# Kernel optimization log

Hardware: AMD Instinct MI355X
Metric: run time of the kernel (lower is better)

## Reference

```python
import jax, jax.numpy as jnp
import numpy as np

# Mamba3/SSD selective state-space mixer (scalar-A-per-head SSD recurrence,
# causal depthwise conv on x/B/C, gated RMSNorm, in/out projections).
D_MODEL = 1024
EXPAND = 2
D_INNER = EXPAND * D_MODEL            # 2048
HEADDIM = D_MODEL // 16               # 64  (head_count=16 -> headdim 64)
NHEADS = D_INNER // HEADDIM           # 32
D_STATE = 128
CONV_W = 4
CONV_DIM = D_INNER + 2 * D_STATE      # x, B, C share the conv
D_IN_PROJ = 2 * D_INNER + 2 * D_STATE + NHEADS  # z, x, B, C, dt
EPS = 1e-5


def setup_inputs() -> dict:
    key = jax.random.key(0)
    ks = jax.random.split(key, 8)
    B, L = 4, 2048
    hidden = jax.random.normal(ks[0], (B, L, D_MODEL), dtype=jnp.float32)
    W_in = jax.random.normal(ks[1], (D_MODEL, D_IN_PROJ), dtype=jnp.float32) * 0.02
    conv_w = jax.random.normal(ks[2], (CONV_DIM, CONV_W), dtype=jnp.float32) * 0.2
    conv_b = jnp.zeros((CONV_DIM,), dtype=jnp.float32)
    # dt_bias: inverse-softplus of dt ~ U[1e-3, 0.1]
    dt = jnp.exp(jax.random.uniform(ks[3], (NHEADS,)) * (np.log(0.1) - np.log(1e-3)) + np.log(1e-3))
    dt_bias = dt + jnp.log(-jnp.expm1(-dt))
    A_log = jnp.log(jax.random.uniform(ks[4], (NHEADS,), minval=1.0, maxval=16.0))
    D = jnp.ones((NHEADS,), dtype=jnp.float32)
    norm_w = jnp.ones((D_INNER,), dtype=jnp.float32)
    W_out = jax.random.normal(ks[5], (D_INNER, D_MODEL), dtype=jnp.float32) * 0.02
    return {"hidden": hidden, "W_in": W_in, "conv_w": conv_w, "conv_b": conv_b,
            "dt_bias": dt_bias, "A_log": A_log, "D": D, "norm_w": norm_w, "W_out": W_out}


def _silu(x):
    return x * jax.nn.sigmoid(x)


def _mixer(hidden, W_in, conv_w, conv_b, dt_bias, A_log, D, norm_w, W_out):
    Bsz, L, _ = hidden.shape
    zxbcdt = hidden @ W_in                                    # [B,L,D_IN_PROJ]
    z = zxbcdt[..., :D_INNER]
    xBC = zxbcdt[..., D_INNER:D_INNER + CONV_DIM]
    dt = zxbcdt[..., -NHEADS:]                                # [B,L,H]
    # causal depthwise conv, width 4 (small fixed loop over taps)
    xp = jnp.pad(xBC, ((0, 0), (CONV_W - 1, 0), (0, 0)))
    conv = sum(xp[:, k:k + L, :] * conv_w[:, k] for k in range(CONV_W))
    xBC = _silu(conv + conv_b)
    x = xBC[..., :D_INNER].reshape(Bsz, L, NHEADS, HEADDIM)   # [B,L,H,P]
    Bm = xBC[..., D_INNER:D_INNER + D_STATE]                  # [B,L,N]
    Cm = xBC[..., D_INNER + D_STATE:]                         # [B,L,N]
    dt = jax.nn.softplus(dt + dt_bias)                        # [B,L,H]
    dA = jnp.exp(dt * (-jnp.exp(A_log)))                      # [B,L,H] decay in (0,1)
    dBx = jnp.einsum('blh,bln,blhp->blhpn', dt, Bm, x)        # [B,L,H,P,N]

    def step(h, inp):
        dA_t, dBx_t, C_t = inp                                # [B,H],[B,H,P,N],[B,N]
        h = dA_t[:, :, None, None] * h + dBx_t
        y = jnp.einsum('bhpn,bn->bhp', h, C_t)
        return h, y

    h0 = jnp.zeros((Bsz, NHEADS, HEADDIM, D_STATE), dtype=hidden.dtype)
    xs = (jnp.moveaxis(dA, 1, 0), jnp.moveaxis(dBx, 1, 0), jnp.moveaxis(Cm, 1, 0))
    _, ys = jax.lax.scan(step, h0, xs)                        # [L,B,H,P]
    y = jnp.moveaxis(ys, 0, 1) + D[None, None, :, None] * x   # skip term
    y = y.reshape(Bsz, L, D_INNER)
    # gated RMSNorm: norm(y * silu(z))
    y = y * _silu(z)
    y = y * jax.lax.rsqrt(jnp.mean(y * y, axis=-1, keepdims=True) + EPS) * norm_w
    return y @ W_out


def reference(hidden, W_in, conv_w, conv_b, dt_bias, A_log, D, norm_w, W_out):
    return _mixer(hidden, W_in, conv_w, conv_b, dt_bias, A_log, D, norm_w, W_out)
```

## Files before the change

### kernel.cpp

```cpp
#include <hip/hip_runtime.h>
#include <math.h>

#define BSZ 4
#define LEN 2048
#define DM 1024
#define DI 2048
#define HD 64
#define NH 32
#define DS 128
#define CD 2304
#define DP 4384
#define NTOK (BSZ*LEN)
#define QCH 128
#define NCH (LEN/QCH)
#define TOFF (DP-NH)

#define CONV_R 64
#define NRB (NTOK/CONV_R)
#define NPAD 4352

typedef unsigned short ushort_t;
typedef __bf16 bf16x8 __attribute__((ext_vector_type(8)));
typedef ushort_t us8 __attribute__((ext_vector_type(8)));
typedef float f32x4 __attribute__((ext_vector_type(4)));

__device__ __forceinline__ ushort_t f2bf(float f) {
    unsigned u = __float_as_uint(f);
    unsigned r = (u + 0x7FFFu + ((u >> 16) & 1u)) >> 16;
    return (ushort_t)r;
}
__device__ __forceinline__ float bf2f(ushort_t u) {
    return __uint_as_float(((unsigned)u) << 16);
}
__device__ __forceinline__ bf16x8 us2bf(us8 v) {
    union { us8 u; bf16x8 b; } x; x.u = v; return x.b;
}

__device__ __forceinline__ void gl_lds16(const void* g, void* l) {
    __builtin_amdgcn_global_load_lds(
        (const __attribute__((address_space(1))) void*)g,
        (__attribute__((address_space(3))) void*)l, 16, 0, 0);
}

__global__ __launch_bounds__(256) void cvt_bf16(
    const float* __restrict__ A, ushort_t* __restrict__ Ab)
{
    size_t i = ((size_t)blockIdx.x * 256 + threadIdx.x) * 4;
    float4 v = *(const float4*)(A + i);
    ushort_t o[4] = { f2bf(v.x), f2bf(v.y), f2bf(v.z), f2bf(v.w) };
    *(uint2*)(Ab + i) = *(uint2*)o;
}

__global__ __launch_bounds__(256) void transpose_cvt(
    const float* __restrict__ W, ushort_t* __restrict__ Wt,
    const float* __restrict__ colscale, int K, int N, int ldw)
{
    __shared__ float T[32][33];
    const int n0 = blockIdx.x * 32;
    const int k0 = blockIdx.y * 32;
    const int tid = threadIdx.x;
    #pragma unroll
    for (int l = 0; l < 4; l++) {
        int idx = tid + l * 256;
        int ki = idx >> 5, nj = idx & 31;
        int n = n0 + nj;
        float s = colscale ? colscale[k0 + ki] : 1.f;
        T[ki][nj] = (n < N) ? W[(size_t)(k0 + ki) * ldw + n] * s : 0.f;
    }
    __syncthreads();
    #pragma unroll
    for (int l = 0; l < 4; l++) {
        int idx = tid + l * 256;
        int nj = idx >> 5, ki = idx & 31;
        Wt[(size_t)(n0 + nj) * K + k0 + ki] = f2bf(T[ki][nj]);
    }
}

template <bool OB>
__global__ __launch_bounds__(256) void gemm_bf16(
    const ushort_t* __restrict__ A, const ushort_t* __restrict__ Bt,
    void* __restrict__ Cp, const float* __restrict__ rowscale,
    int K, int lda, int ldb, int ldc, int nmax)
{
    __shared__ __align__(16) ushort_t As[128 * 32];
    __shared__ __align__(16) ushort_t Bs[128 * 32];
    const int tid = threadIdx.x;
    int bid = blockIdx.y * gridDim.x + blockIdx.x;
    const int nwg = gridDim.x * gridDim.y;
    if (!(nwg & 7)) bid = (bid & 7) * (nwg >> 3) + (bid >> 3);
    const int n0 = (bid % gridDim.x) * 128;
    const int m0 = (bid / gridDim.x) * 128;
    const int lane = tid & 63;
    const int w = tid >> 6;
    const int wm = w >> 1, wn = w & 1;
    const int lm = lane & 15, quad = lane >> 4;

    const int srow = tid >> 2;
    const int skq = (tid & 3) * 8;
    const ushort_t* ga0 = A + (size_t)(m0 + srow) * lda + skq;
    const ushort_t* ga1 = A + (size_t)(m0 + 64 + srow) * lda + skq;
    const ushort_t* gb0 = Bt + (size_t)(n0 + srow) * ldb + skq;
    const ushort_t* gb1 = Bt + (size_t)(n0 + 64 + srow) * ldb + skq;
    ushort_t* la0 = &As[srow * 32 + skq];
    ushort_t* la1 = &As[(64 + srow) * 32 + skq];
    ushort_t* lb0 = &Bs[srow * 32 + skq];
    ushort_t* lb1 = &Bs[(64 + srow) * 32 + skq];

    f32x4 acc[4][4];
    #pragma unroll
    for (int i = 0; i < 4; i++)
        #pragma unroll
        for (int j = 0; j < 4; j++) acc[i][j] = (f32x4){0.f, 0.f, 0.f, 0.f};

    for (int k0 = 0; k0 < K; k0 += 32) {
        gl_lds16(ga0, la0);
        gl_lds16(ga1, la1);
        gl_lds16(gb0, lb0);
        gl_lds16(gb1, lb1);
        ga0 += 32; ga1 += 32; gb0 += 32; gb1 += 32;
        __syncthreads();
        bf16x8 af[4], bfr[4];
        #pragma unroll
        for (int i = 0; i < 4; i++)
            af[i] = *(const bf16x8*)&As[(wm * 64 + i * 16 + lm) * 32 + quad * 8];
        #pragma unroll
        for (int j = 0; j < 4; j++)
            bfr[j] = *(const bf16x8*)&Bs[(wn * 64 + j * 16 + lm) * 32 + quad * 8];
        #pragma unroll
        for (int i = 0; i < 4; i++)
            #pragma unroll
            for (int j = 0; j < 4; j++)
                acc[i][j] = __builtin_amdgcn_mfma_f32_16x16x32_bf16(af[i], bfr[j], acc[i][j], 0, 0, 0);
        __syncthreads();
    }

    #pragma unroll
    for (int i = 0; i < 4; i++) {
        int row = m0 + wm * 64 + i * 16 + quad * 4;
        float rs[4] = {1.f, 1.f, 1.f, 1.f};
        if (rowscale) {
            #pragma unroll
            for (int r = 0; r < 4; r++) rs[r] = rowscale[row + r];
        }
        #pragma unroll
        for (int j = 0; j < 4; j++) {
            int col = n0 + wn * 64 + j * 16 + lm;
            if (col < nmax) {
                #pragma unroll
                for (int r = 0; r < 4; r++) {
                    if (OB)
                        ((ushort_t*)Cp)[(size_t)(row + r) * ldc + col] = f2bf(acc[i][j][r] * rs[r]);
                    else
                        ((float*)Cp)[(size_t)(row + r) * ldc + col] = acc[i][j][r] * rs[r];
                }
            }
        }
    }
}

__global__ __launch_bounds__(256) void conv_silu_bf16(
    const ushort_t* __restrict__ xbcb, const float* __restrict__ cw,
    const float* __restrict__ cb, ushort_t* __restrict__ xT,
    ushort_t* __restrict__ Bn, ushort_t* __restrict__ BT,
    ushort_t* __restrict__ Cn)
{
    __shared__ ushort_t Tl[256][68];
    const int tid = threadIdx.x;
    const int c = blockIdx.x * 256 + tid;
    const int rb = blockIdx.y;
    const int row0 = rb * CONV_R;
    const bool isBC = (blockIdx.x == 8);

    const float w0 = cw[c*4+0], w1 = cw[c*4+1], w2 = cw[c*4+2], w3 = cw[c*4+3];
    const float bias = cb[c];
    float h0 = 0.f, h1 = 0.f, h2 = 0.f;
    if ((row0 & (LEN - 1)) != 0) {
        h0 = bf2f(xbcb[(size_t)(row0 - 3) * NPAD + c]);
        h1 = bf2f(xbcb[(size_t)(row0 - 2) * NPAD + c]);
        h2 = bf2f(xbcb[(size_t)(row0 - 1) * NPAD + c]);
    }
    const ushort_t* p = xbcb + (size_t)row0 * NPAD + c;
    for (int r = 0; r < CONV_R; r++) {
        float xin = bf2f(*p);
        float a = bias + w0*h0 + w1*h1 + w2*h2 + w3*xin;
        ushort_t bv = f2bf(a / (1.f + __expf(-a)));
        Tl[tid][r] = bv;
        if (isBC) {
            int row = row0 + r;
            if (tid < DS) Bn[(size_t)row * DS + tid] = bv;
            else          Cn[(size_t)row * DS + (tid - DS)] = bv;
        }
        h0 = h1; h1 = h2; h2 = xin;
        p += NPAD;
    }
    __syncthreads();

    const int seg = tid & 7;
    const int clb = tid >> 3;
    if (!isBC) {
        #pragma unroll
        for (int pass = 0; pass < 8; pass++) {
            int cl = pass * 32 + clb;
            int cc = blockIdx.x * 256 + cl;
            us8 v;
            #pragma unroll
            for (int j = 0; j < 8; j++) v[j] = Tl[cl][seg * 8 + j];
            *(us8*)&xT[(size_t)cc * NTOK + row0 + seg * 8] = v;
        }
    } else {
        #pragma unroll
        for (int pass = 0; pass < 4; pass++) {
            int n = pass * 32 + clb;
            us8 v;
            #pragma unroll
            for (int j = 0; j < 8; j++) v[j] = Tl[n][seg * 8 + j];
            *(us8*)&BT[(size_t)n * NTOK + row0 + seg * 8] = v;
        }
    }
}

__global__ __launch_bounds__(256) void gct_gemm(
    const ushort_t* __restrict__ Bn, const ushort_t* __restrict__ Cn,
    float* __restrict__ Graw)
{
    const int bc = blockIdx.x;
    const int chunk = bc % NCH;
    const int b = bc / NCH;
    const size_t rowbase = (size_t)b * LEN + (size_t)chunk * QCH;
    const int tid = threadIdx.x;
    const int w = tid >> 6, lane = tid & 63;
    const int lm = lane & 15, quad = lane >> 4;
    const int tw0 = w * 32;

    f32x4 acc[2][8];
    #pragma unroll
    for (int ti = 0; ti < 2; ti++)
        #pragma unroll
        for (int sj = 0; sj < 8; sj++) acc[ti][sj] = (f32x4){0.f, 0.f, 0.f, 0.f};

    #pragma unroll
    for (int ks = 0; ks < 4; ks++) {
        const int k0 = ks * 32 + quad * 8;
        bf16x8 a0 = *(const bf16x8*)&Cn[(rowbase + tw0 + lm) * DS + k0];
        bf16x8 a1 = *(const bf16x8*)&Cn[(rowbase + tw0 + 16 + lm) * DS + k0];
        #pragma unroll
        for (int sj = 0; sj < 8; sj++) {
            bf16x8 bb = *(const bf16x8*)&Bn[(rowbase + sj * 16 + lm) * DS + k0];
            acc[0][sj] = __builtin_amdgcn_mfma_f32_16x16x32_bf16(a0, bb, acc[0][sj], 0, 0, 0);
            acc[1][sj] = __builtin_amdgcn_mfma_f32_16x16x32_bf16(a1, bb, acc[1][sj], 0, 0, 0);
        }
    }
    float* G = Graw + (size_t)bc * (QCH * QCH);
    #pragma unroll
    for (int ti = 0; ti < 2; ti++)
        #pragma unroll
        for (int sj = 0; sj < 8; sj++)
            #pragma unroll
            for (int r = 0; r < 4; r++)
                G[(size_t)(tw0 + ti * 16 + quad * 4 + r) * QCH + sj * 16 + lm] = acc[ti][sj][r];
}

__global__ __launch_bounds__(256) void dt_proc_fp32(
    const float* __restrict__ hidden, const float* __restrict__ W_in,
    const float* __restrict__ dt_bias, const float* __restrict__ A_log,
    float* __restrict__ dtv, float* __restrict__ ldA)
{
    const int h = threadIdx.x & 31;
    const int tt = threadIdx.x >> 5;
    const int t = blockIdx.x * 8 + tt;
    const float* hr = hidden + (size_t)t * DM;
    const float* wc = W_in + TOFF + h;
    float a0 = 0.f, a1 = 0.f, a2 = 0.f, a3 = 0.f;
    for (int k = 0; k < DM; k += 4) {
        a0 += hr[k+0] * wc[(size_t)(k+0) * DP];
        a1 += hr[k+1] * wc[(size_t)(k+1) * DP];
        a2 += hr[k+2] * wc[(size_t)(k+2) * DP];
        a3 += hr[k+3] * wc[(size_t)(k+3) * DP];
    }
    float v = (a0 + a1) + (a2 + a3) + dt_bias[h];
    float sp = (v > 20.f) ? v : log1pf(expf(v));
    int idx = t * NH + h;
    dtv[idx] = sp;
    ldA[idx] = -sp * expf(A_log[h]);
}

__global__ __launch_bounds__(64) void scan_chunk(
    const float* __restrict__ dtv, const float* __restrict__ ldA,
    float* __restrict__ lcpb, float* __restrict__ dtsb,
    float* __restrict__ coefb, float* __restrict__ csum)
{
    const int blk = blockIdx.x;
    const int chunk = blk % NCH;
    const int bh = blk / NCH;
    const int h = bh % NH;
    const int b = bh / NH;
    const int lane = threadIdx.x;
    const size_t rowbase = (size_t)b * LEN + (size_t)chunk * QCH;
    const int t0 = 2 * lane, t1 = 2 * lane + 1;
    float v0 = ldA[(rowbase + t0) * NH + h];
    float v1 = ldA[(rowbase + t1) * NH + h];
    float d0 = dtv[(rowbase + t0) * NH + h];
    float d1 = dtv[(rowbase + t1) * NH + h];
    float pair = v0 + v1;
    #pragma unroll
    for (int off = 1; off < 64; off <<= 1) {
        float n = __shfl_up(pair, off, 64);
        if (lane >= off) pair += n;
    }
    float l1 = pair, l0 = pair - v1;
    float total = __shfl(pair, 63, 64);
    size_t base = (size_t)blk * QCH;
    *(float2*)&lcpb[base + t0] = make_float2(l0, l1);
    *(float2*)&dtsb[base + t0] = make_float2(d0, d1);
    *(float2*)&coefb[base + t0] =
        make_float2(__expf(total - l0) * d0, __expf(total - l1) * d1);
    if (lane == 63) csum[blk] = total;
}

__global__ __launch_bounds__(256) void phase1_mfma(
    const ushort_t* __restrict__ xT, const ushort_t* __restrict__ BT,
    const float* __restrict__ coefb, float* __restrict__ S)
{
    const int h = blockIdx.x & (NH - 1);
    const int bc = blockIdx.x >> 5;
    const int chunk = bc % NCH;
    const int b = bc / NCH;
    const int blko = (b * NH + h) * NCH + chunk;
    const int tid = threadIdx.x;
    const size_t rowbase = (size_t)b * LEN + (size_t)chunk * QCH;

    __shared__ float coef[QCH];
    if (tid < QCH) coef[tid] = coefb[(size_t)blko * QCH + tid];
    __syncthreads();

    const int w = tid >> 6, lane = tid & 63;
    const int lm = lane & 15, quad = lane >> 4;
    const int nw0 = w * 32;

    f32x4 acc[4][2];
    #pragma unroll
    for (int i = 0; i < 4; i++)
        #pragma unroll
        for (int j = 0; j < 2; j++) acc[i][j] = (f32x4){0.f, 0.f, 0.f, 0.f};

    #pragma unroll
    for (int ks = 0; ks < 4; ks++) {
        const int k0 = ks * 32 + quad * 8;
        bf16x8 a[4];
        #pragma unroll
        for (int mi = 0; mi < 4; mi++)
            a[mi] = *(const bf16x8*)&xT[(size_t)(h * HD + mi * 16 + lm) * NTOK + rowbase + k0];
        float cf[8];
        #pragma unroll
        for (int j = 0; j < 8; j++) cf[j] = coef[k0 + j];
        #pragma unroll
        for (int ni = 0; ni < 2; ni++) {
            us8 raw = *(const us8*)&BT[(size_t)(nw0 + ni * 16 + lm) * NTOK + rowbase + k0];
            us8 sb;
            #pragma unroll
            for (int j = 0; j < 8; j++) sb[j] = f2bf(bf2f(raw[j]) * cf[j]);
            bf16x8 bfr = us2bf(sb);
            __builtin_amdgcn_s_setprio(1);
            #pragma unroll
            for (int mi = 0; mi < 4; mi++)
                acc[mi][ni] = __builtin_amdgcn_mfma_f32_16x16x32_bf16(a[mi], bfr, acc[mi][ni], 0, 0, 0);
            __builtin_amdgcn_s_setprio(0);
        }
    }
    float* Sb = S + (size_t)blko * (HD * DS);
    #pragma unroll
    for (int mi = 0; mi < 4; mi++)
        #pragma unroll
        for (int ni = 0; ni < 2; ni++)
            #pragma unroll
            for (int r = 0; r < 4; r++)
                Sb[(size_t)(mi * 16 + quad * 4 + r) * DS + nw0 + ni * 16 + lm] = acc[mi][ni][r];
}

__global__ __launch_bounds__(256) void phase2(
    const float* __restrict__ S, const float* __restrict__ csum,
    ushort_t* __restrict__ hsb)
{
    const int bh = blockIdx.x >> 3;
    const int esl = blockIdx.x & 7;
    const int tid = threadIdx.x;
    const int eb = esl * 1024 + tid;
    float run[4] = {0.f, 0.f, 0.f, 0.f};
    for (int c = 0; c < NCH; c++) {
        float P = __expf(csum[bh * NCH + c]);
        size_t base = (size_t)(bh * NCH + c) * (HD * DS);
        #pragma unroll
        for (int i = 0; i < 4; i++) {
            size_t idx = base + eb + i * 256;
            float s = S[idx];
            hsb[idx] = f2bf(run[i]);
            run[i] = P * run[i] + s;
        }
    }
}

__global__ __launch_bounds__(256) void phase3_mfma(
    const ushort_t* __restrict__ xT, const ushort_t* __restrict__ Cn,
    const ushort_t* __restrict__ hsb, const float* __restrict__ Graw,
    const float* __restrict__ lcpb, const float* __restrict__ dtsb,
    const float* __restrict__ Dvec, ushort_t* __restrict__ zxb,
    float* __restrict__ ss)
{
    const int tid = threadIdx.x;
    const int h = blockIdx.x & (NH - 1);
    const int bc = blockIdx.x >> 5;
    const int chunk = bc % NCH;
    const int b = bc / NCH;
    const int blko = (b * NH + h) * NCH + chunk;
    const size_t rowbase = (size_t)b * LEN + (size_t)chunk * QCH;

    __shared__ float lcp[QCH];
    __shared__ float dts[QCH];
    if (tid < QCH) {
        lcp[tid] = lcpb[(size_t)blko * QCH + tid];
        dts[tid] = dtsb[(size_t)blko * QCH + tid];
    }
    __syncthreads();

    const int w = tid >> 6, lane = tid & 63;
    const int lm = lane & 15, quad = lane >> 4;
    const int tw0 = w * 32;

    const float* Gr = Graw + (size_t)bc * (QCH * QCH);
    const ushort_t* hsp = hsb + (size_t)blko * (HD * DS);

    f32x4 acc2[2][4];
    #pragma unroll
    for (int ti = 0; ti < 2; ti++)
        #pragma unroll
        for (int pi = 0; pi < 4; pi++) acc2[ti][pi] = (f32x4){0.f, 0.f, 0.f, 0.f};

    #pragma unroll
    for (int ks = 0; ks < 8; ks++) {
        bf16x8 a[2], bb[4];
        if (ks < 4) {
            const int k0 = ks * 32 + quad * 8;
            #pragma unroll
            for (int ti = 0; ti < 2; ti++) {
                int t = tw0 + ti * 16 + lm;
                float lt = lcp[t];
                const float* gp = Gr + (size_t)t * QCH + k0;
                float4 g0 = *(const float4*)gp;
                float4 g1 = *(const float4*)(gp + 4);
                float ge[8] = { g0.x, g0.y, g0.z, g0.w, g1.x, g1.y, g1.z, g1.w };
                us8 sb;
                #pragma unroll
                for (int j = 0; j < 8; j++) {
                    int s = k0 + j;
                    float wv = (s <= t) ? (__expf(lt - lcp[s]) * dts[s]) : 0.f;
                    sb[j] = f2bf(ge[j] * wv);
                }
                a[ti] = us2bf(sb);
            }
            #pragma unroll
            for (int pi = 0; pi < 4; pi++)
                bb[pi] = *(const bf16x8*)&xT[(size_t)(h * HD + pi * 16 + lm) * NTOK + rowbase + k0];
        } else {
            const int k0 = (ks - 4) * 32 + quad * 8;
            #pragma unroll
            for (int ti = 0; ti < 2; ti++) {
                int t = tw0 + ti * 16 + lm;
                float sc = __expf(lcp[t]);
                us8 raw = *(const us8*)&Cn[(rowbase + t) * DS + k0];
                us8 sb;
                #pragma unroll
                for (int j = 0; j < 8; j++) sb[j] = f2bf(bf2f(raw[j]) * sc);
                a[ti] = us2bf(sb);
            }
            #pragma unroll
            for (int pi = 0; pi < 4; pi++)
                bb[pi] = *(const bf16x8*)&hsp[(size_t)(pi * 16 + lm) * DS + k0];
        }
        __builtin_amdgcn_s_setprio(1);
        #pragma unroll
        for (int ti = 0; ti < 2; ti++)
            #pragma unroll
            for (int pi = 0; pi < 4; pi++)
                acc2[ti][pi] = __builtin_amdgcn_mfma_f32_16x16x32_bf16(a[ti], bb[pi], acc2[ti][pi], 0, 0, 0);
        __builtin_amdgcn_s_setprio(0);
    }

    const float Dh = Dvec[h];
    float vsq[2][4] = {};
    #pragma unroll
    for (int ti = 0; ti < 2; ti++)
        #pragma unroll
        for (int pi = 0; pi < 4; pi++) {
            int tb = tw0 + ti * 16 + quad * 4;
            int col = h * HD + pi * 16 + lm;
            ushort4 xv = *(const ushort4*)&xT[(size_t)(h * HD + pi * 16 + lm) * NTOK + rowbase + tb];
            const ushort_t* xe = (const ushort_t*)&xv;
            #pragma unroll
            for (int r = 0; r < 4; r++) {
                size_t grow = rowbase + tb + r;
                float y = acc2[ti][pi][r] + Dh * bf2f(xe[r]);
                float z = bf2f(zxb[grow * NPAD + col]);
                float v = y * (z / (1.f + __expf(-z)));
                vsq[ti][r] += v * v;
                zxb[grow * NPAD + DI + col] = f2bf(v);
            }
        }
    #pragma unroll
    for (int ti = 0; ti < 2; ti++)
        #pragma unroll
        for (int r = 0; r < 4; r++) {
            float s = vsq[ti][r];
            s += __shfl_xor(s, 1, 64);
            s += __shfl_xor(s, 2, 64);
            s += __shfl_xor(s, 4, 64);
            s += __shfl_xor(s, 8, 64);
            if (lm == 0) {
                int tb = tw0 + ti * 16 + quad * 4 + r;
                atomicAdd(&ss[rowbase + tb], s);
            }
        }
}

__global__ __launch_bounds__(256) void rms_finalize(
    const float* __restrict__ ss, float* __restrict__ rr)
{
    int t = blockIdx.x * 256 + threadIdx.x;
    rr[t] = rsqrtf(ss[t] * (1.f / DI) + 1e-5f);
}

extern "C" void kernel_launch(void* const* d_in, const int* in_sizes, int n_in,
                              void* d_out, int out_size, void* d_ws, size_t ws_size,
                              hipStream_t stream)
{
    const float* hidden  = (const float*)d_in[0];
    const float* W_in    = (const float*)d_in[1];
    const float* conv_w  = (const float*)d_in[2];
    const float* conv_b  = (const float*)d_in[3];
    const float* dt_bias = (const float*)d_in[4];
    const float* A_log   = (const float*)d_in[5];
    const float* Dv      = (const float*)d_in[6];
    const float* norm_w  = (const float*)d_in[7];
    const float* W_out   = (const float*)d_in[8];
    float* out = (float*)d_out;

    char* ws = (char*)d_ws;
    size_t o = 0;
    ushort_t* zxb  = (ushort_t*)(ws + o); o += (size_t)NTOK * NPAD * 2;
    float* S       = (float*)(ws + o);    o += (size_t)BSZ * NH * NCH * HD * DS * 4;
    ushort_t* xT   = (ushort_t*)(ws + o); o += (size_t)DI * NTOK * 2;
    ushort_t* Bn   = (ushort_t*)(ws + o); o += (size_t)NTOK * DS * 2;
    ushort_t* BT   = (ushort_t*)(ws + o); o += (size_t)DS * NTOK * 2;
    ushort_t* Cn   = (ushort_t*)(ws + o); o += (size_t)NTOK * DS * 2;
    ushort_t* hsb  = (ushort_t*)(ws + o); o += (size_t)BSZ * NH * NCH * HD * DS * 2;
    float* Graw    = (float*)(ws + o);    o += (size_t)BSZ * NCH * QCH * QCH * 4;
    float* dtv     = (float*)(ws + o);    o += (size_t)NTOK * NH * 4;
    float* ldA     = (float*)(ws + o);    o += (size_t)NTOK * NH * 4;
    float* lcpb    = (float*)(ws + o);    o += (size_t)BSZ * NH * LEN * 4;
    float* dtsb    = (float*)(ws + o);    o += (size_t)BSZ * NH * LEN * 4;
    float* coefb   = (float*)(ws + o);    o += (size_t)BSZ * NH * LEN * 4;
    float* csum    = (float*)(ws + o);    o += (size_t)BSZ * NH * NCH * 4;
    float* ss      = (float*)(ws + o);    o += (size_t)NTOK * 4;
    float* rr      = (float*)(ws + o);    o += (size_t)NTOK * 4;
    ushort_t* Ah   = (ushort_t*)S;
    ushort_t* W1t  = (ushort_t*)((char*)S + (size_t)NTOK * DM * 2);
    ushort_t* Wot  = hsb;
    ushort_t* xbcb = zxb + DI;
    ushort_t* ynb  = zxb + DI;

    hipMemsetAsync(ss, 0, (size_t)NTOK * 4, stream);
    cvt_bf16<<<(NTOK * DM) / 1024, 256, 0, stream>>>(hidden, Ah);
    transpose_cvt<<<dim3(NPAD / 32, DM / 32), 256, 0, stream>>>(
        W_in, W1t, nullptr, DM, NPAD, DP);
    gemm_bf16<true><<<dim3(NPAD / 128, NTOK / 128), 256, 0, stream>>>(
        Ah, W1t, zxb, nullptr, DM, DM, DM, NPAD, NPAD);
    conv_silu_bf16<<<dim3(CD / 256, NRB), 256, 0, stream>>>(
        xbcb, conv_w, conv_b, xT, Bn, BT, Cn);
    gct_gemm<<<BSZ * NCH, 256, 0, stream>>>(Bn, Cn, Graw);
    dt_proc_fp32<<<NTOK / 8, 256, 0, stream>>>(hidden, W_in, dt_bias, A_log, dtv, ldA);
    scan_chunk<<<BSZ * NH * NCH, 64, 0, stream>>>(dtv, ldA, lcpb, dtsb, coefb, csum);
    phase1_mfma<<<BSZ * NH * NCH, 256, 0, stream>>>(xT, BT, coefb, S);
    phase2<<<BSZ * NH * 8, 256, 0, stream>>>(S, csum, hsb);
    phase3_mfma<<<BSZ * NH * NCH, 256, 0, stream>>>(
        xT, Cn, hsb, Graw, lcpb, dtsb, Dv, zxb, ss);
    rms_finalize<<<NTOK / 256, 256, 0, stream>>>(ss, rr);
    transpose_cvt<<<dim3(DM / 32, DI / 32), 256, 0, stream>>>(
        W_out, Wot, norm_w, DI, DM, DM);
    gemm_bf16<false><<<dim3(DM / 128, NTOK / 128), 256, 0, stream>>>(
        ynb, Wot, out, rr, DI, NPAD, DI, DM, DM);
}
```

Measured before the change: 531.7 us.

## Replace input-projection GEMM with 256x256-tile, 512-thread double-buffered MFMA kernel

Adds a new bf16 GEMM kernel for the input projection. It uses 256x256 output tiles, 8 waves per block, K-step 64 and double-buffered LDS loads issued asynchronously, and raises wave priority around the MFMA bursts. Larger tiles raise arithmetic intensity and cut global traffic per FLOP, while the prefetch overlaps loads with compute. The cost is higher LDS use (128KB double-buffered) and more registers, which lowers occupancy. The grid drops to 17x32 blocks, so wave quantization on the CUs may suffer.

```diff
diff --git a/kernel.cpp b/kernel.cpp
--- a/kernel.cpp
+++ b/kernel.cpp
@@ -73,6 +73,115 @@
         int idx = tid + l * 256;
         int nj = idx >> 5, ki = idx & 31;
         Wt[(size_t)(n0 + nj) * K + k0 + ki] = f2bf(T[ki][nj]);
+    }
+}
+
+__global__ __launch_bounds__(512, 2) void gemm1_256(
+    const ushort_t* __restrict__ A, const ushort_t* __restrict__ Bt,
+    ushort_t* __restrict__ C, int K, int lda, int ldb, int ldc)
+{
+    __shared__ __align__(16) ushort_t LA[2][2][128 * 64];
+    __shared__ __align__(16) ushort_t LB[2][2][128 * 64];
+    const int tid = threadIdx.x;
+    int bid = blockIdx.y * gridDim.x + blockIdx.x;
+    const int nwg = gridDim.x * gridDim.y;
+    if (!(nwg & 7)) bid = (bid & 7) * (nwg >> 3) + (bid >> 3);
+    const int n0 = (bid % gridDim.x) * 256;
+    const int m0 = (bid / gridDim.x) * 256;
+    const int lane = tid & 63;
+    const int w = tid >> 6;
+    const int wm = w >> 2, wn = w & 3;
+    const int lm = lane & 15, quad = lane >> 4;
+    const int swz = ((lm >> 2) & 1) << 5;
+    const int ck0 = ((0 * 64 + quad * 16) ^ swz) >> 1;
+    const int ck1 = ((1 * 64 + quad * 16) ^ swz) >> 1;
+
+    const int srow = tid >> 3;
+    const int scolb = ((tid & 7) * 16) ^ (((tid >> 5) & 1) << 5);
+    const char* gA = (const char*)A + ((size_t)(m0 + srow) * lda) * 2 + scolb;
+    const char* gB = (const char*)Bt + ((size_t)(n0 + srow) * ldb) * 2 + scolb;
+    const size_t strA = (size_t)64 * lda * 2;
+    const size_t strB = (size_t)64 * ldb * 2;
+    const int ldst = tid * 8;
+
+    f32x4 acc[8][4];
+    #pragma unroll
+    for (int i = 0; i < 8; i++)
+        #pragma unroll
+        for (int j = 0; j < 4; j++) acc[i][j] = (f32x4){0.f, 0.f, 0.f, 0.f};
+
+    const int NTt = K >> 6;
+
+    {
+        const char* a = gA;
+        const char* b = gB;
+        #pragma unroll
+        for (int i = 0; i < 4; i++)
+            gl_lds16(a + i * strA, &LA[0][i >> 1][(i & 1) * 4096 + ldst]);
+        #pragma unroll
+        for (int i = 0; i < 4; i++)
+            gl_lds16(b + i * strB, &LB[0][i >> 1][(i & 1) * 4096 + ldst]);
+    }
+    __syncthreads();
+
+    for (int kt = 0; kt < NTt; ++kt) {
+        const int cur = kt & 1;
+        if (kt + 1 < NTt) {
+            const char* a = gA + (size_t)(kt + 1) * 128;
+            const char* b = gB + (size_t)(kt + 1) * 128;
+            const int nxt = cur ^ 1;
+            #pragma unroll
+            for (int i = 0; i < 4; i++)
+                gl_lds16(a + i * strA, &LA[nxt][i >> 1][(i & 1) * 4096 + ldst]);
+            #pragma unroll
+            for (int i = 0; i < 4; i++)
+                gl_lds16(b + i * strB, &LB[nxt][i >> 1][(i & 1) * 4096 + ldst]);
+        }
+        #pragma unroll
+        for (int mq = 0; mq < 2; mq++) {
+            bf16x8 af[4][2];
+            #pragma unroll
+            for (int m4 = 0; m4 < 4; m4++) {
+                const int rbase = ((mq * 4 + m4) * 16 + lm) << 6;
+                af[m4][0] = *(const bf16x8*)&LA[cur][wm][rbase + ck0];
+                af[m4][1] = *(const bf16x8*)&LA[cur][wm][rbase + ck1];
+            }
+            #pragma unroll
+            for (int nq = 0; nq < 2; nq++) {
+                bf16x8 bfr[2][2];
+                #pragma unroll
+                for (int n2 = 0; n2 < 2; n2++) {
+                    const int rbase = ((wn & 1) * 64 + (nq * 2 + n2) * 16 + lm) << 6;
+                    bfr[n2][0] = *(const bf16x8*)&LB[cur][wn >> 1][rbase + ck0];
+                    bfr[n2][1] = *(const bf16x8*)&LB[cur][wn >> 1][rbase + ck1];
+                }
+                __builtin_amdgcn_s_setprio(1);
+                #pragma unroll
+                for (int kk = 0; kk < 2; kk++)
+                    #pragma unroll
+                    for (int m4 = 0; m4 < 4; m4++)
+                        #pragma unroll
+                        for (int n2 = 0; n2 < 2; n2++)
+                            acc[mq * 4 + m4][nq * 2 + n2] =
+                                __builtin_amdgcn_mfma_f32_16x16x32_bf16(
+                                    af[m4][kk], bfr[n2][kk],
+                                    acc[mq * 4 + m4][nq * 2 + n2], 0, 0, 0);
+                __builtin_amdgcn_s_setprio(0);
+            }
+        }
+        if (kt + 1 < NTt) __syncthreads();
+    }
+
+    #pragma unroll
+    for (int mf = 0; mf < 8; mf++) {
+        const int row = m0 + wm * 128 + mf * 16 + quad * 4;
+        #pragma unroll
+        for (int nf = 0; nf < 4; nf++) {
+            const int col = n0 + wn * 64 + nf * 16 + lm;
+            #pragma unroll
+            for (int r = 0; r < 4; r++)
+                C[(size_t)(row + r) * ldc + col] = f2bf(acc[mf][nf][r]);
+        }
     }
 }
 
@@ -571,8 +680,8 @@
     cvt_bf16<<<(NTOK * DM) / 1024, 256, 0, stream>>>(hidden, Ah);
     transpose_cvt<<<dim3(NPAD / 32, DM / 32), 256, 0, stream>>>(
         W_in, W1t, nullptr, DM, NPAD, DP);
-    gemm_bf16<true><<<dim3(NPAD / 128, NTOK / 128), 256, 0, stream>>>(
-        Ah, W1t, zxb, nullptr, DM, DM, DM, NPAD, NPAD);
+    gemm1_256<<<dim3(NPAD / 256, NTOK / 256), 512, 0, stream>>>(
+        Ah, W1t, zxb, DM, DM, DM, NPAD);
     conv_silu_bf16<<<dim3(CD / 256, NRB), 256, 0, stream>>>(
         xbcb, conv_w, conv_b, xT, Bn, BT, Cn);
     gct_gemm<<<BSZ * NCH, 256, 0, stream>>>(Bn, Cn, Graw);
```

Result: no change. 541.1 us (+1.8%).

## Double-buffer GEMM tiles with K=64 stages, swizzled LDS and prefetch

Applied to the files above, without the earlier changes.

Rewrites the bf16 GEMM main loop to use double-buffered 128x64 LDS tiles. Direct-to-LDS loads for the next K tile are issued before computing the current one, overlapping memory with MFMA and halving the barriers per K. An XOR swizzle on the LDS columns is meant to avoid bank conflicts. It also drops the column bounds check and raises wave priority around the MFMA block, at the cost of four times the LDS footprint, which may reduce occupancy.

```diff
diff --git a/kernel.cpp b/kernel.cpp
--- a/kernel.cpp
+++ b/kernel.cpp
@@ -77,13 +77,13 @@
 }
 
 template <bool OB>
-__global__ __launch_bounds__(256) void gemm_bf16(
+__global__ __launch_bounds__(256) void gemm128(
     const ushort_t* __restrict__ A, const ushort_t* __restrict__ Bt,
     void* __restrict__ Cp, const float* __restrict__ rowscale,
-    int K, int lda, int ldb, int ldc, int nmax)
-{
-    __shared__ __align__(16) ushort_t As[128 * 32];
-    __shared__ __align__(16) ushort_t Bs[128 * 32];
+    int K, int lda, int ldb, int ldc)
+{
+    __shared__ __align__(16) ushort_t LA[2][128 * 64];
+    __shared__ __align__(16) ushort_t LB[2][128 * 64];
     const int tid = threadIdx.x;
     int bid = blockIdx.y * gridDim.x + blockIdx.x;
     const int nwg = gridDim.x * gridDim.y;
@@ -94,17 +94,17 @@
     const int w = tid >> 6;
     const int wm = w >> 1, wn = w & 1;
     const int lm = lane & 15, quad = lane >> 4;
-
-    const int srow = tid >> 2;
-    const int skq = (tid & 3) * 8;
-    const ushort_t* ga0 = A + (size_t)(m0 + srow) * lda + skq;
-    const ushort_t* ga1 = A + (size_t)(m0 + 64 + srow) * lda + skq;
-    const ushort_t* gb0 = Bt + (size_t)(n0 + srow) * ldb + skq;
-    const ushort_t* gb1 = Bt + (size_t)(n0 + 64 + srow) * ldb + skq;
-    ushort_t* la0 = &As[srow * 32 + skq];
-    ushort_t* la1 = &As[(64 + srow) * 32 + skq];
-    ushort_t* lb0 = &Bs[srow * 32 + skq];
-    ushort_t* lb1 = &Bs[(64 + srow) * 32 + skq];
+    const int swz = (lm & 7) << 4;
+    const int ck0 = ((0 * 64 + quad * 16) ^ swz) >> 1;
+    const int ck1 = ((1 * 64 + quad * 16) ^ swz) >> 1;
+
+    const int srow = tid >> 3;
+    const int scolb = ((tid & 7) * 16) ^ ((srow & 7) << 4);
+    const char* gA = (const char*)A + ((size_t)(m0 + srow) * lda) * 2 + scolb;
+    const char* gB = (const char*)Bt + ((size_t)(n0 + srow) * ldb) * 2 + scolb;
+    const size_t strA = (size_t)32 * lda * 2;
+    const size_t strB = (size_t)32 * ldb * 2;
+    const int ldst = tid * 8;
 
     f32x4 acc[4][4];
     #pragma unroll
@@ -112,47 +112,74 @@
         #pragma unroll
         for (int j = 0; j < 4; j++) acc[i][j] = (f32x4){0.f, 0.f, 0.f, 0.f};
 
-    for (int k0 = 0; k0 < K; k0 += 32) {
-        gl_lds16(ga0, la0);
-        gl_lds16(ga1, la1);
-        gl_lds16(gb0, lb0);
-        gl_lds16(gb1, lb1);
-        ga0 += 32; ga1 += 32; gb0 += 32; gb1 += 32;
-        __syncthreads();
-        bf16x8 af[4], bfr[4];
-        #pragma unroll
-        for (int i = 0; i < 4; i++)
-            af[i] = *(const bf16x8*)&As[(wm * 64 + i * 16 + lm) * 32 + quad * 8];
+    const int NTt = K >> 6;
+
+    auto STAGE = [&](int kt1, int nxt) {
+        const char* a = gA + (size_t)kt1 * 128;
+        const char* b = gB + (size_t)kt1 * 128;
         #pragma unroll
         for (int j = 0; j < 4; j++)
-            bfr[j] = *(const bf16x8*)&Bs[(wn * 64 + j * 16 + lm) * 32 + quad * 8];
-        #pragma unroll
-        for (int i = 0; i < 4; i++)
-            #pragma unroll
-            for (int j = 0; j < 4; j++)
-                acc[i][j] = __builtin_amdgcn_mfma_f32_16x16x32_bf16(af[i], bfr[j], acc[i][j], 0, 0, 0);
-        __syncthreads();
-    }
-
-    #pragma unroll
-    for (int i = 0; i < 4; i++) {
-        int row = m0 + wm * 64 + i * 16 + quad * 4;
+            gl_lds16(a + j * strA, &LA[nxt][j * 2048 + ldst]);
+        #pragma unroll
+        for (int j = 0; j < 4; j++)
+            gl_lds16(b + j * strB, &LB[nxt][j * 2048 + ldst]);
+    };
+
+    STAGE(0, 0);
+
+    for (int kt = 0; kt < NTt; ++kt) {
+        const int cur = kt & 1;
+        __builtin_amdgcn_s_barrier();
+        if (kt + 1 < NTt) {
+            STAGE(kt + 1, cur ^ 1);
+            asm volatile("s_waitcnt vmcnt(8)" ::: "memory");
+        } else {
+            asm volatile("s_waitcnt vmcnt(0)" ::: "memory");
+        }
+        __builtin_amdgcn_s_barrier();
+
+        bf16x8 af[4][2], bf[4][2];
+        #pragma unroll
+        for (int s = 0; s < 4; s++) {
+            const int rb = (wm * 64 + s * 16 + lm) << 6;
+            af[s][0] = *(const bf16x8*)&LA[cur][rb + ck0];
+            af[s][1] = *(const bf16x8*)&LA[cur][rb + ck1];
+        }
+        #pragma unroll
+        for (int t = 0; t < 4; t++) {
+            const int rb = (wn * 64 + t * 16 + lm) << 6;
+            bf[t][0] = *(const bf16x8*)&LB[cur][rb + ck0];
+            bf[t][1] = *(const bf16x8*)&LB[cur][rb + ck1];
+        }
+        __builtin_amdgcn_s_setprio(1);
+        #pragma unroll
+        for (int kk = 0; kk < 2; kk++)
+            #pragma unroll
+            for (int s = 0; s < 4; s++)
+                #pragma unroll
+                for (int t = 0; t < 4; t++)
+                    acc[s][t] = __builtin_amdgcn_mfma_f32_16x16x32_bf16(
+                        af[s][kk], bf[t][kk], acc[s][t], 0, 0, 0);
+        __builtin_amdgcn_s_setprio(0);
+    }
+
+    #pragma unroll
+    for (int s = 0; s < 4; s++) {
+        const int row = m0 + wm * 64 + s * 16 + quad * 4;
         float rs[4] = {1.f, 1.f, 1.f, 1.f};
-        if (rowscale) {
+        if (!OB && rowscale) {
             #pragma unroll
             for (int r = 0; r < 4; r++) rs[r] = rowscale[row + r];
         }
         #pragma unroll
-        for (int j = 0; j < 4; j++) {
-            int col = n0 + wn * 64 + j * 16 + lm;
-            if (col < nmax) {
-                #pragma unroll
-                for (int r = 0; r < 4; r++) {
-                    if (OB)
-                        ((ushort_t*)Cp)[(size_t)(row + r) * ldc + col] = f2bf(acc[i][j][r] * rs[r]);
-                    else
-                        ((float*)Cp)[(size_t)(row + r) * ldc + col] = acc[i][j][r] * rs[r];
-                }
+        for (int t = 0; t < 4; t++) {
+            const int col = n0 + wn * 64 + t * 16 + lm;
+            #pragma unroll
+            for (int r = 0; r < 4; r++) {
+                if (OB)
+                    ((ushort_t*)Cp)[(size_t)(row + r) * ldc + col] = f2bf(acc[s][t][r]);
+                else
+                    ((float*)Cp)[(size_t)(row + r) * ldc + col] = acc[s][t][r] * rs[r];
             }
         }
     }
@@ -571,8 +598,8 @@
     cvt_bf16<<<(NTOK * DM) / 1024, 256, 0, stream>>>(hidden, Ah);
     transpose_cvt<<<dim3(NPAD / 32, DM / 32), 256, 0, stream>>>(
         W_in, W1t, nullptr, DM, NPAD, DP);
-    gemm_bf16<true><<<dim3(NPAD / 128, NTOK / 128), 256, 0, stream>>>(
-        Ah, W1t, zxb, nullptr, DM, DM, DM, NPAD, NPAD);
+    gemm128<true><<<dim3(NPAD / 128, NTOK / 128), 256, 0, stream>>>(
+        Ah, W1t, zxb, nullptr, DM, DM, DM, NPAD);
     conv_silu_bf16<<<dim3(CD / 256, NRB), 256, 0, stream>>>(
         xbcb, conv_w, conv_b, xT, Bn, BT, Cn);
     gct_gemm<<<BSZ * NCH, 256, 0, stream>>>(Bn, Cn, Graw);
@@ -585,6 +612,6 @@
     rms_finalize<<<NTOK / 256, 256, 0, stream>>>(ss, rr);
     transpose_cvt<<<dim3(DM / 32, DI / 32), 256, 0, stream>>>(
         W_out, Wot, norm_w, DI, DM, DM);
-    gemm_bf16<false><<<dim3(DM / 128, NTOK / 128), 256, 0, stream>>>(
-        ynb, Wot, out, rr, DI, NPAD, DI, DM, DM);
-}
+    gemm128<false><<<dim3(DM / 128, NTOK / 128), 256, 0, stream>>>(
+        ynb, Wot, out, rr, DI, NPAD, DI, DM);
+}
```

New measurement: 507.2 us. -4.6%, faster.
